# Kernel tuning notes

Hardware: AMD Instinct MI355X
Metric: run time of the kernel (lower is better)

## Reference

```python
import jax, jax.numpy as jnp
import numpy as np

FEAT_DIM = 80
FLOOR = 1e-06


def setup_inputs() -> dict:
    key = jax.random.key(0)
    k_x, = jax.random.split(key, 1)
    B, F, T = 32, FEAT_DIM, 6000
    # non-negative spectrogram-like energies
    x = jax.random.uniform(k_x, (B, F, T), dtype=jnp.float32)
    smooth = jnp.full((F,), 0.04, dtype=jnp.float32)
    alpha = jnp.full((F,), 0.96, dtype=jnp.float32)
    delta = jnp.full((F,), 2.0, dtype=jnp.float32)
    root = jnp.full((F,), 2.0, dtype=jnp.float32)
    return {"tensor": x, "smooth": smooth, "alpha": alpha, "delta": delta, "root": root}


def _pcen(x, smooth, alpha, delta, root):
    # x: [B, F, T]; params: [F]
    s = jnp.clip(smooth, 0.0, 1.0)  # [F]
    xT = jnp.moveaxis(x, -1, 0)     # [T, B, F]

    def step(carry, xt):
        m = (1.0 - s) * carry + s * xt  # broadcast [F] over [B, F]
        return m, m

    _, ema_rest = jax.lax.scan(step, xT[0], xT[1:])
    ema = jnp.concatenate([xT[:1], ema_rest], axis=0)  # [T, B, F]
    ema = jnp.moveaxis(ema, 0, -1)                      # [B, F, T]

    a = jnp.minimum(alpha, 1.0)[:, None]  # [F, 1]
    r = jnp.maximum(root, 1.0)[:, None]   # [F, 1]
    d = delta[:, None]                    # [F, 1]
    one_over_r = 1.0 / r
    return (x / (FLOOR + ema) ** a + d) ** one_over_r - d ** one_over_r


def reference(tensor, smooth, alpha, delta, root):
    return _pcen(tensor, smooth, alpha, delta, root)
```

## Files before the change

### kernel.cpp

```cpp
#include <hip/hip_runtime.h>
#include <hip/hip_bf16.h>

#define T_LEN   6000
#define F_DIM   80
#define NROWS   2560
#define CHUNK   256
#define NCHUNK  24
#define DEPTH   8
#define FLOORV  1e-6f

__device__ __forceinline__ float hw_exp2(float x) { return __builtin_amdgcn_exp2f(x); }
__device__ __forceinline__ float hw_log2(float x) { return __builtin_amdgcn_logf(x); }

__device__ __forceinline__ float4 load_chunk(const float* __restrict__ p, int k, int lane) {
    int t = k * CHUNK + lane * 4;
    if (t < T_LEN) {
        return *reinterpret_cast<const float4*>(p + t);
    }
    return make_float4(0.f, 0.f, 0.f, 0.f);
}

__device__ __forceinline__ float pcen_elem(float x, float m, float neg_a, float d,
                                           float inv_r, float droot) {
    float g = hw_exp2(neg_a * hw_log2(m + FLOORV));
    float y = fmaf(x, g, d);
    return hw_exp2(inv_r * hw_log2(y)) - droot;
}

__global__ __launch_bounds__(256) void pcen_kernel(
    const float* __restrict__ x,
    const float* __restrict__ smooth,
    const float* __restrict__ alpha,
    const float* __restrict__ delta,
    const float* __restrict__ root,
    float* __restrict__ out)
{
    const int lane = threadIdx.x & 63;
    const int wave = threadIdx.x >> 6;
    const int row  = blockIdx.x * 4 + wave;
    if (row >= NROWS) return;
    const int f = row % F_DIM;

    float s   = fminf(fmaxf(smooth[f], 0.f), 1.f);
    float c   = 1.f - s;
    float a   = fminf(alpha[f], 1.f);
    float d   = delta[f];
    float r   = fmaxf(root[f], 1.f);
    float inv_r = 1.f / r;
    float neg_a = -a;
    float droot = hw_exp2(inv_r * hw_log2(d));

    const float c1 = c, c2 = c * c, c3 = c2 * c, c4 = c2 * c2;
    float q0 = c4;
    float q1 = q0 * q0;
    float q2 = q1 * q1;
    float q3 = q2 * q2;
    float q4 = q3 * q3;
    float q5 = q4 * q4;
    float c256 = q5 * q5;
    float c4lane = (lane == 0) ? 1.0f : hw_exp2(4.0f * (float)lane * hw_log2(c));

    const float* __restrict__ px = x   + (size_t)row * T_LEN;
    float*       __restrict__ po = out + (size_t)row * T_LEN;

    float4 v[DEPTH];
#pragma unroll
    for (int i = 0; i < DEPTH; ++i) v[i] = load_chunk(px, i, lane);

    float carry = px[0];

#pragma unroll
    for (int k = 0; k < NCHUNK; ++k) {
        float4 cur = v[k % DEPTH];
        if (k + DEPTH < NCHUNK) v[k % DEPTH] = load_chunk(px, k + DEPTH, lane);

        float b0 = s * cur.x;
        float b1 = fmaf(c, b0, s * cur.y);
        float b2 = fmaf(c, b1, s * cur.z);
        float b3 = fmaf(c, b2, s * cur.w);

        float B = b3;
        {
            float Bu;
            Bu = __shfl_up(B, 1, 64);  if (lane >= 1)  B = fmaf(q0, Bu, B);
            Bu = __shfl_up(B, 2, 64);  if (lane >= 2)  B = fmaf(q1, Bu, B);
            Bu = __shfl_up(B, 4, 64);  if (lane >= 4)  B = fmaf(q2, Bu, B);
            Bu = __shfl_up(B, 8, 64);  if (lane >= 8)  B = fmaf(q3, Bu, B);
            Bu = __shfl_up(B, 16, 64); if (lane >= 16) B = fmaf(q4, Bu, B);
            Bu = __shfl_up(B, 32, 64); if (lane >= 32) B = fmaf(q5, Bu, B);
        }
        float Bex = __shfl_up(B, 1, 64);
        if (lane == 0) Bex = 0.f;
        float m_in = fmaf(c4lane, carry, Bex);

        float B63 = __shfl(B, 63, 64);
        carry = fmaf(c256, carry, B63);

        float m0 = fmaf(c1, m_in, b0);
        float m1 = fmaf(c2, m_in, b1);
        float m2 = fmaf(c3, m_in, b2);
        float m3 = fmaf(c4, m_in, b3);

        float4 o;
        o.x = pcen_elem(cur.x, m0, neg_a, d, inv_r, droot);
        o.y = pcen_elem(cur.y, m1, neg_a, d, inv_r, droot);
        o.z = pcen_elem(cur.z, m2, neg_a, d, inv_r, droot);
        o.w = pcen_elem(cur.w, m3, neg_a, d, inv_r, droot);

        int t = k * CHUNK + lane * 4;
        if (t < T_LEN) {
            *reinterpret_cast<float4*>(po + t) = o;
        }
    }
}

extern "C" void kernel_launch(void* const* d_in, const int* in_sizes, int n_in,
                              void* d_out, int out_size, void* d_ws, size_t ws_size,
                              hipStream_t stream) {
    const float* x      = (const float*)d_in[0];
    const float* smooth = (const float*)d_in[1];
    const float* alpha  = (const float*)d_in[2];
    const float* delta  = (const float*)d_in[3];
    const float* root   = (const float*)d_in[4];
    float* out = (float*)d_out;

    dim3 grid(NROWS / 4);
    dim3 block(256);
    pcen_kernel<<<grid, block, 0, stream>>>(x, smooth, alpha, delta, root, out);
}
```

Before: 115.9 us.

## Use nontemporal loads/stores, one-wave blocks, and sqrt fast path for root

Switches global loads and stores to nontemporal builtins so the streaming data bypasses cache retention. Launches one 64-thread block per row instead of four waves per block, which changes scheduling granularity. Adds a runtime branch that uses sqrt instead of an exp2/log2 pair when 1/root equals 0.5. The sqrt path is still correct for that parameter value, but the branch adds a small per-element uniform check.

```diff
diff --git a/kernel.cpp b/kernel.cpp
--- a/kernel.cpp
+++ b/kernel.cpp
@@ -9,25 +9,20 @@
 #define DEPTH   8
 #define FLOORV  1e-6f
 
+typedef float vfloat4 __attribute__((ext_vector_type(4)));
+
 __device__ __forceinline__ float hw_exp2(float x) { return __builtin_amdgcn_exp2f(x); }
 __device__ __forceinline__ float hw_log2(float x) { return __builtin_amdgcn_logf(x); }
 
-__device__ __forceinline__ float4 load_chunk(const float* __restrict__ p, int k, int lane) {
+__device__ __forceinline__ vfloat4 load_chunk(const float* __restrict__ p, int k, int lane) {
     int t = k * CHUNK + lane * 4;
     if (t < T_LEN) {
-        return *reinterpret_cast<const float4*>(p + t);
+        return __builtin_nontemporal_load(reinterpret_cast<const vfloat4*>(p + t));
     }
-    return make_float4(0.f, 0.f, 0.f, 0.f);
+    return (vfloat4){0.f, 0.f, 0.f, 0.f};
 }
 
-__device__ __forceinline__ float pcen_elem(float x, float m, float neg_a, float d,
-                                           float inv_r, float droot) {
-    float g = hw_exp2(neg_a * hw_log2(m + FLOORV));
-    float y = fmaf(x, g, d);
-    return hw_exp2(inv_r * hw_log2(y)) - droot;
-}
-
-__global__ __launch_bounds__(256) void pcen_kernel(
+__global__ __launch_bounds__(64) void pcen_kernel(
     const float* __restrict__ x,
     const float* __restrict__ smooth,
     const float* __restrict__ alpha,
@@ -35,10 +30,8 @@
     const float* __restrict__ root,
     float* __restrict__ out)
 {
-    const int lane = threadIdx.x & 63;
-    const int wave = threadIdx.x >> 6;
-    const int row  = blockIdx.x * 4 + wave;
-    if (row >= NROWS) return;
+    const int lane = threadIdx.x;
+    const int row  = blockIdx.x;
     const int f = row % F_DIM;
 
     float s   = fminf(fmaxf(smooth[f], 0.f), 1.f);
@@ -48,7 +41,8 @@
     float r   = fmaxf(root[f], 1.f);
     float inv_r = 1.f / r;
     float neg_a = -a;
-    float droot = hw_exp2(inv_r * hw_log2(d));
+    const bool use_sqrt = (inv_r == 0.5f);
+    float droot = use_sqrt ? __builtin_sqrtf(d) : hw_exp2(inv_r * hw_log2(d));
 
     const float c1 = c, c2 = c * c, c3 = c2 * c, c4 = c2 * c2;
     float q0 = c4;
@@ -63,7 +57,7 @@
     const float* __restrict__ px = x   + (size_t)row * T_LEN;
     float*       __restrict__ po = out + (size_t)row * T_LEN;
 
-    float4 v[DEPTH];
+    vfloat4 v[DEPTH];
 #pragma unroll
     for (int i = 0; i < DEPTH; ++i) v[i] = load_chunk(px, i, lane);
 
@@ -71,7 +65,7 @@
 
 #pragma unroll
     for (int k = 0; k < NCHUNK; ++k) {
-        float4 cur = v[k % DEPTH];
+        vfloat4 cur = v[k % DEPTH];
         if (k + DEPTH < NCHUNK) v[k % DEPTH] = load_chunk(px, k + DEPTH, lane);
 
         float b0 = s * cur.x;
@@ -96,20 +90,28 @@
         float B63 = __shfl(B, 63, 64);
         carry = fmaf(c256, carry, B63);
 
-        float m0 = fmaf(c1, m_in, b0);
-        float m1 = fmaf(c2, m_in, b1);
-        float m2 = fmaf(c3, m_in, b2);
-        float m3 = fmaf(c4, m_in, b3);
+        float m[4];
+        m[0] = fmaf(c1, m_in, b0);
+        m[1] = fmaf(c2, m_in, b1);
+        m[2] = fmaf(c3, m_in, b2);
+        m[3] = fmaf(c4, m_in, b3);
 
-        float4 o;
-        o.x = pcen_elem(cur.x, m0, neg_a, d, inv_r, droot);
-        o.y = pcen_elem(cur.y, m1, neg_a, d, inv_r, droot);
-        o.z = pcen_elem(cur.z, m2, neg_a, d, inv_r, droot);
-        o.w = pcen_elem(cur.w, m3, neg_a, d, inv_r, droot);
+        float xin[4] = {cur.x, cur.y, cur.z, cur.w};
+        vfloat4 o;
+        float ov[4];
+#pragma unroll
+        for (int j = 0; j < 4; ++j) {
+            float g = hw_exp2(neg_a * hw_log2(m[j] + FLOORV));
+            float y = fmaf(xin[j], g, d);
+            float p = use_sqrt ? __builtin_sqrtf(y)
+                               : hw_exp2(inv_r * hw_log2(y));
+            ov[j] = p - droot;
+        }
+        o.x = ov[0]; o.y = ov[1]; o.z = ov[2]; o.w = ov[3];
 
         int t = k * CHUNK + lane * 4;
         if (t < T_LEN) {
-            *reinterpret_cast<float4*>(po + t) = o;
+            __builtin_nontemporal_store(o, reinterpret_cast<vfloat4*>(po + t));
         }
     }
 }
@@ -124,7 +126,7 @@
     const float* root   = (const float*)d_in[4];
     float* out = (float*)d_out;
 
-    dim3 grid(NROWS / 4);
-    dim3 block(256);
+    dim3 grid(NROWS);
+    dim3 block(64);
     pcen_kernel<<<grid, block, 0, stream>>>(x, smooth, alpha, delta, root, out);
 }
```

After: 125.6 us. +8.3%, slower.
